# Kernel tuning notes

Hardware: AMD Instinct MI355X
Metric: run time of the kernel (lower is better)

## Reference

```python
import jax, jax.numpy as jnp
import numpy as np

N = 50000
E = 800000
IN_F = 128
OUT_F = 64
HEADS = 4
NEG_SLOPE = 0.2
EPS = 1e-8


def setup_inputs() -> dict:
    key = jax.random.key(0)
    k1, k2, k3, k4, k5 = jax.random.split(key, 5)
    x = jax.random.normal(k1, (N, IN_F), dtype=jnp.float32)
    edge_index = jax.random.randint(k2, (2, E), 0, N, dtype=jnp.int64)
    # xavier-uniform-like scales
    wb = float(np.sqrt(6.0 / (IN_F + OUT_F)))
    ab = float(np.sqrt(6.0 / (OUT_F + 1)))
    W = jax.random.uniform(k3, (HEADS, IN_F, OUT_F), dtype=jnp.float32, minval=-wb, maxval=wb)
    a_src = jax.random.uniform(k4, (HEADS, OUT_F, 1), dtype=jnp.float32, minval=-ab, maxval=ab)
    a_dst = jax.random.uniform(k5, (HEADS, OUT_F, 1), dtype=jnp.float32, minval=-ab, maxval=ab)
    return {"x": x, "edge_index": edge_index, "W": W, "a_src": a_src, "a_dst": a_dst}


def reference(x, edge_index, W, a_src, a_dst):
    n = x.shape[0]
    src, dst = edge_index[0], edge_index[1]
    # per-head projection: (H, N, F)
    Wh = jnp.einsum('ni,hif->hnf', x, W)
    e_src = jnp.einsum('hnf,hf->hn', Wh, a_src[..., 0])
    e_dst = jnp.einsum('hnf,hf->hn', Wh, a_dst[..., 0])
    e = jax.nn.leaky_relu(e_src[:, src] + e_dst[:, dst], NEG_SLOPE)  # (H, E)
    # edge softmax over destination; original initializes e_max to zeros,
    # so effective max is max(segment_max, 0)
    seg_max = jax.vmap(lambda eh: jax.ops.segment_max(eh, dst, num_segments=n))(e)
    e_max = jnp.maximum(seg_max, 0.0)
    exp_e = jnp.exp(e - e_max[:, dst])
    exp_sum = jax.vmap(lambda ee: jax.ops.segment_sum(ee, dst, num_segments=n))(exp_e)
    att = exp_e / (exp_sum[:, dst] + EPS)  # (H, E); dropout omitted (eval)
    # weighted scatter-add aggregation: (H, E, F) messages -> (H, N, F)
    msgs = att[..., None] * Wh[:, src]
    out = jax.vmap(lambda m: jax.ops.segment_sum(m, dst, num_segments=n))(msgs)
    # concat heads: (N, H*F)
    return out.transpose(1, 0, 2).reshape(n, -1)
```

## Files before the change

kernel.cpp:

```cpp
#include <hip/hip_runtime.h>
#include <hip/hip_bf16.h>

#define N_NODES 50000
#define E_EDGES 800000
#define IN_F    128
#define OUT_F   64
#define HEADS   4
#define HF      (HEADS * OUT_F)
#define NEG_SLOPE 0.2f
#define EPS     1e-8f
#define CAP     64
#define NB_INIT ((N_NODES + 255) / 256)

typedef __attribute__((ext_vector_type(8))) short bf16x8;
typedef __attribute__((ext_vector_type(4))) float f32x4;

__device__ __forceinline__ unsigned short f2bf(float f) {
    return __hip_bfloat16_raw(__float2bfloat16(f)).x;
}
__device__ __forceinline__ float bf2f(unsigned short u) {
    return __uint_as_float((unsigned)u << 16);
}

__global__ __launch_bounds__(256) void wcvt_kernel(
    const float* __restrict__ W,
    short* __restrict__ Wtb,
    int* __restrict__ cnt)
{
    const int i = blockIdx.x * 256 + threadIdx.x;
    if (i < N_NODES) cnt[i] = 0;
    if (i < HEADS * IN_F * OUT_F) {
        const int h  = i >> 13;
        const int fl = (i >> 7) & 63;
        const int k  = i & 127;
        Wtb[i] = (short)f2bf(W[h * (IN_F * OUT_F) + k * OUT_F + fl]);
    }
}

__global__ __launch_bounds__(256) void proj_kernel(
    const float* __restrict__ x,
    const short* __restrict__ Wtb,
    const float* __restrict__ a_src,
    const float* __restrict__ a_dst,
    const int* __restrict__ src,
    const int* __restrict__ dst,
    unsigned short* __restrict__ Whb,
    float* __restrict__ esrc,
    float* __restrict__ edst,
    int* __restrict__ cnt,
    int* __restrict__ csr)
{
    __shared__ short xs[16][136];
    __shared__ unsigned short ot[4][16][72];

    const int tid = threadIdx.x;
    const int n0 = blockIdx.x * 16;

    const int e  = blockIdx.x * 256 + tid;
    const int de = dst[e];
    const int se = src[e];

    {
        const int row = tid >> 4;
        const int kb = (tid & 15) * 8;
        const float* xp = x + (size_t)(n0 + row) * IN_F + kb;
        const float4 x0 = *(const float4*)(xp);
        const float4 x1 = *(const float4*)(xp + 4);
        bf16x8 v;
        v[0] = (short)f2bf(x0.x); v[1] = (short)f2bf(x0.y);
        v[2] = (short)f2bf(x0.z); v[3] = (short)f2bf(x0.w);
        v[4] = (short)f2bf(x1.x); v[5] = (short)f2bf(x1.y);
        v[6] = (short)f2bf(x1.z); v[7] = (short)f2bf(x1.w);
        *(bf16x8*)&xs[row][kb] = v;
    }
    __syncthreads();

    const int pos = atomicAdd(&cnt[de], 1);

    const int h = tid >> 6;
    const int lane = tid & 63;
    const int c = lane & 15;
    const int quad = lane >> 4;

    bf16x8 a[4];
#pragma unroll
    for (int ks = 0; ks < 4; ++ks)
        a[ks] = *(const bf16x8*)&xs[c][ks * 32 + quad * 8];

    f32x4 acc[4];
#pragma unroll
    for (int nt = 0; nt < 4; ++nt) acc[nt] = (f32x4){0.f, 0.f, 0.f, 0.f};

    const short* Wh_head = Wtb + (h << 13);
#pragma unroll
    for (int nt = 0; nt < 4; ++nt) {
        const short* wrow = Wh_head + ((nt * 16 + c) << 7) + (quad << 3);
#pragma unroll
        for (int ks = 0; ks < 4; ++ks) {
            const bf16x8 b = *(const bf16x8*)(wrow + (ks << 5));
            acc[nt] = __builtin_amdgcn_mfma_f32_16x16x32_bf16(a[ks], b, acc[nt], 0, 0, 0);
        }
    }

    float ps[4] = {0.f, 0.f, 0.f, 0.f};
    float pd[4] = {0.f, 0.f, 0.f, 0.f};
#pragma unroll
    for (int nt = 0; nt < 4; ++nt) {
        const float as = a_src[h * OUT_F + nt * 16 + c];
        const float ad = a_dst[h * OUT_F + nt * 16 + c];
#pragma unroll
        for (int r = 0; r < 4; ++r) {
            ps[r] += acc[nt][r] * as;
            pd[r] += acc[nt][r] * ad;
        }
    }
#pragma unroll
    for (int m = 1; m < 16; m <<= 1) {
#pragma unroll
        for (int r = 0; r < 4; ++r) {
            ps[r] += __shfl_xor(ps[r], m);
            pd[r] += __shfl_xor(pd[r], m);
        }
    }
    if (c == 0) {
#pragma unroll
        for (int r = 0; r < 4; ++r) {
            const int n = n0 + quad * 4 + r;
            esrc[n * HEADS + h] = ps[r];
            edst[n * HEADS + h] = pd[r];
        }
    }

#pragma unroll
    for (int nt = 0; nt < 4; ++nt) {
#pragma unroll
        for (int r = 0; r < 4; ++r)
            ot[h][quad * 4 + r][nt * 16 + c] = f2bf(acc[nt][r]);
    }
    {
        const int row = lane >> 2;
        const int co  = (lane & 3) * 16;
        unsigned short* gp = Whb + (size_t)(n0 + row) * HF + h * OUT_F + co;
        const unsigned short* sp = &ot[h][row][co];
        *(int4*)(gp)     = *(const int4*)(sp);
        *(int4*)(gp + 8) = *(const int4*)(sp + 8);
    }

    if (pos < CAP) __builtin_nontemporal_store(se, &csr[de * CAP + pos]);
}

__global__ __launch_bounds__(256) void aggregate_kernel(
    const int* __restrict__ cnt,
    const int* __restrict__ csr,
    const float* __restrict__ esrc,
    const float* __restrict__ edst,
    const unsigned short* __restrict__ Whb,
    float* __restrict__ out)
{
    __shared__ int   sb[4][64];
    __shared__ float pb[4][64][4];

    const int wid = threadIdx.x >> 6;
    const int lane = threadIdx.x & 63;
    const int d = blockIdx.x * 4 + wid;

    int deg = cnt[d];
    deg = deg > CAP ? CAP : deg;

    const float4 ed4 = *(const float4*)(edst + d * HEADS);
    const int h = lane >> 4;
    const unsigned short* wbase = Whb + (lane << 2);

    float l0 = 0.f, l1 = 0.f, l2 = 0.f, l3 = 0.f;
    if (lane < deg) {
        const int s = __builtin_nontemporal_load(&csr[d * CAP + lane]);
        const float4 es4 = *(const float4*)(esrc + s * HEADS);
        float v0 = es4.x + ed4.x; v0 = v0 > 0.f ? v0 : NEG_SLOPE * v0;
        float v1 = es4.y + ed4.y; v1 = v1 > 0.f ? v1 : NEG_SLOPE * v1;
        float v2 = es4.z + ed4.z; v2 = v2 > 0.f ? v2 : NEG_SLOPE * v2;
        float v3 = es4.w + ed4.w; v3 = v3 > 0.f ? v3 : NEG_SLOPE * v3;
        l0 = __expf(v0); l1 = __expf(v1); l2 = __expf(v2); l3 = __expf(v3);
        sb[wid][lane] = s;
        *(float4*)pb[wid][lane] = (float4){l0, l1, l2, l3};
    }

    float o0 = 0.f, o1 = 0.f, o2 = 0.f, o3 = 0.f;
    int i = 0;
    for (; i + 8 <= deg; i += 8) {
        int s[8];
#pragma unroll
        for (int j = 0; j < 8; ++j) s[j] = sb[wid][i + j];
        ushort4 w[8];
#pragma unroll
        for (int j = 0; j < 8; ++j)
            w[j] = *(const ushort4*)(wbase + (unsigned)s[j] * HF);
        float q[8];
#pragma unroll
        for (int j = 0; j < 8; ++j) q[j] = pb[wid][i + j][h];
#pragma unroll
        for (int j = 0; j < 8; ++j) {
            o0 += q[j] * bf2f(w[j].x);
            o1 += q[j] * bf2f(w[j].y);
            o2 += q[j] * bf2f(w[j].z);
            o3 += q[j] * bf2f(w[j].w);
        }
    }
    for (; i < deg; ++i) {
        const int s0 = sb[wid][i];
        const float q0 = pb[wid][i][h];
        const ushort4 w0 = *(const ushort4*)(wbase + (unsigned)s0 * HF);
        o0 += q0 * bf2f(w0.x);
        o1 += q0 * bf2f(w0.y);
        o2 += q0 * bf2f(w0.z);
        o3 += q0 * bf2f(w0.w);
    }

#pragma unroll
    for (int m = 1; m < 64; m <<= 1) {
        l0 += __shfl_xor(l0, m);
        l1 += __shfl_xor(l1, m);
        l2 += __shfl_xor(l2, m);
        l3 += __shfl_xor(l3, m);
    }
    const float lsum = (h == 0) ? l0 : (h == 1) ? l1 : (h == 2) ? l2 : l3;
    const float r = 1.f / (lsum + EPS);

    const f32x4 o4 = {o0 * r, o1 * r, o2 * r, o3 * r};
    __builtin_nontemporal_store(o4, (f32x4*)(out + (size_t)d * HF + (lane << 2)));
}

extern "C" void kernel_launch(void* const* d_in, const int* in_sizes, int n_in,
                              void* d_out, int out_size, void* d_ws, size_t ws_size,
                              hipStream_t stream) {
    const float* x      = (const float*)d_in[0];
    const int*   eidx   = (const int*)d_in[1];
    const float* W      = (const float*)d_in[2];
    const float* a_src  = (const float*)d_in[3];
    const float* a_dst  = (const float*)d_in[4];
    float* out = (float*)d_out;

    const int* src = eidx;
    const int* dst = eidx + E_EDGES;

    unsigned short* Whb = (unsigned short*)d_ws;
    float* esrc   = (float*)(Whb + (size_t)N_NODES * HF);
    float* edst   = esrc + (size_t)N_NODES * HEADS;
    int*   cnt    = (int*)(edst + (size_t)N_NODES * HEADS);
    int*   csr    = cnt + N_NODES;
    short* Wtb    = (short*)(csr + (size_t)N_NODES * CAP);

    wcvt_kernel<<<NB_INIT, 256, 0, stream>>>(W, Wtb, cnt);

    proj_kernel<<<N_NODES / 16, 256, 0, stream>>>(x, Wtb, a_src, a_dst, src, dst,
                                                  Whb, esrc, edst, cnt, csr);

    aggregate_kernel<<<N_NODES / 4, 256, 0, stream>>>(cnt, csr, esrc, edst, Whb, out);
}
```

Baseline: 193.1 us.

## Pad degree counters, store 16-bit CSR indices, unroll aggregation by 16

Each per-node degree counter now sits in its own 64-byte slot, so atomics on different nodes do not share cache lines. CSR source indices are stored as 16-bit values, which halves that buffer's footprint and relies on the node count fitting in 16 bits. The aggregation gather loop handles 16 neighbours per step with zero-padded shared entries instead of an 8-wide loop plus a tail loop, giving more loads in flight. The trade-offs are a larger counter array to zero, scattered sub-dword stores, and wasted gathers for low-degree nodes.

```diff
diff --git a/kernel.cpp b/kernel.cpp
--- a/kernel.cpp
+++ b/kernel.cpp
@@ -28,7 +28,11 @@
     int* __restrict__ cnt)
 {
     const int i = blockIdx.x * 256 + threadIdx.x;
-    if (i < N_NODES) cnt[i] = 0;
+    if (i < N_NODES) {
+        const int4 z = {0, 0, 0, 0};
+        int4* p = (int4*)(cnt + i * 16);
+        p[0] = z; p[1] = z; p[2] = z; p[3] = z;
+    }
     if (i < HEADS * IN_F * OUT_F) {
         const int h  = i >> 13;
         const int fl = (i >> 7) & 63;
@@ -48,7 +52,7 @@
     float* __restrict__ esrc,
     float* __restrict__ edst,
     int* __restrict__ cnt,
-    int* __restrict__ csr)
+    unsigned short* __restrict__ csr)
 {
     __shared__ short xs[16][136];
     __shared__ unsigned short ot[4][16][72];
@@ -75,7 +79,7 @@
     }
     __syncthreads();
 
-    const int pos = atomicAdd(&cnt[de], 1);
+    const int pos = atomicAdd(&cnt[de << 4], 1);
 
     const int h = tid >> 6;
     const int lane = tid & 63;
@@ -146,12 +150,13 @@
         *(int4*)(gp + 8) = *(const int4*)(sp + 8);
     }
 
-    if (pos < CAP) __builtin_nontemporal_store(se, &csr[de * CAP + pos]);
+    if (pos < CAP)
+        __builtin_nontemporal_store((unsigned short)se, &csr[(size_t)de * CAP + pos]);
 }
 
 __global__ __launch_bounds__(256) void aggregate_kernel(
     const int* __restrict__ cnt,
-    const int* __restrict__ csr,
+    const unsigned short* __restrict__ csr,
     const float* __restrict__ esrc,
     const float* __restrict__ edst,
     const unsigned short* __restrict__ Whb,
@@ -164,7 +169,7 @@
     const int lane = threadIdx.x & 63;
     const int d = blockIdx.x * 4 + wid;
 
-    int deg = cnt[d];
+    int deg = cnt[d << 4];
     deg = deg > CAP ? CAP : deg;
 
     const float4 ed4 = *(const float4*)(edst + d * HEADS);
@@ -172,47 +177,41 @@
     const unsigned short* wbase = Whb + (lane << 2);
 
     float l0 = 0.f, l1 = 0.f, l2 = 0.f, l3 = 0.f;
+    int sfill = 0;
+    float4 pfill = {0.f, 0.f, 0.f, 0.f};
     if (lane < deg) {
-        const int s = __builtin_nontemporal_load(&csr[d * CAP + lane]);
+        const int s = (int)__builtin_nontemporal_load(&csr[(size_t)d * CAP + lane]);
         const float4 es4 = *(const float4*)(esrc + s * HEADS);
         float v0 = es4.x + ed4.x; v0 = v0 > 0.f ? v0 : NEG_SLOPE * v0;
         float v1 = es4.y + ed4.y; v1 = v1 > 0.f ? v1 : NEG_SLOPE * v1;
         float v2 = es4.z + ed4.z; v2 = v2 > 0.f ? v2 : NEG_SLOPE * v2;
         float v3 = es4.w + ed4.w; v3 = v3 > 0.f ? v3 : NEG_SLOPE * v3;
         l0 = __expf(v0); l1 = __expf(v1); l2 = __expf(v2); l3 = __expf(v3);
-        sb[wid][lane] = s;
-        *(float4*)pb[wid][lane] = (float4){l0, l1, l2, l3};
-    }
+        sfill = s;
+        pfill = (float4){l0, l1, l2, l3};
+    }
+    sb[wid][lane] = sfill;
+    *(float4*)pb[wid][lane] = pfill;
 
     float o0 = 0.f, o1 = 0.f, o2 = 0.f, o3 = 0.f;
-    int i = 0;
-    for (; i + 8 <= deg; i += 8) {
-        int s[8];
-#pragma unroll
-        for (int j = 0; j < 8; ++j) s[j] = sb[wid][i + j];
-        ushort4 w[8];
-#pragma unroll
-        for (int j = 0; j < 8; ++j)
+    for (int i = 0; i < deg; i += 16) {
+        int s[16];
+#pragma unroll
+        for (int j = 0; j < 16; ++j) s[j] = sb[wid][i + j];
+        ushort4 w[16];
+#pragma unroll
+        for (int j = 0; j < 16; ++j)
             w[j] = *(const ushort4*)(wbase + (unsigned)s[j] * HF);
-        float q[8];
-#pragma unroll
-        for (int j = 0; j < 8; ++j) q[j] = pb[wid][i + j][h];
-#pragma unroll
-        for (int j = 0; j < 8; ++j) {
+        float q[16];
+#pragma unroll
+        for (int j = 0; j < 16; ++j) q[j] = pb[wid][i + j][h];
+#pragma unroll
+        for (int j = 0; j < 16; ++j) {
             o0 += q[j] * bf2f(w[j].x);
             o1 += q[j] * bf2f(w[j].y);
             o2 += q[j] * bf2f(w[j].z);
             o3 += q[j] * bf2f(w[j].w);
         }
-    }
-    for (; i < deg; ++i) {
-        const int s0 = sb[wid][i];
-        const float q0 = pb[wid][i][h];
-        const ushort4 w0 = *(const ushort4*)(wbase + (unsigned)s0 * HF);
-        o0 += q0 * bf2f(w0.x);
-        o1 += q0 * bf2f(w0.y);
-        o2 += q0 * bf2f(w0.z);
-        o3 += q0 * bf2f(w0.w);
     }
 
 #pragma unroll
@@ -246,7 +245,7 @@
     float* esrc   = (float*)(Whb + (size_t)N_NODES * HF);
     float* edst   = esrc + (size_t)N_NODES * HEADS;
     int*   cnt    = (int*)(edst + (size_t)N_NODES * HEADS);
-    int*   csr    = cnt + N_NODES;
+    unsigned short* csr = (unsigned short*)(cnt + (size_t)N_NODES * 16);
     short* Wtb    = (short*)(csr + (size_t)N_NODES * CAP);
 
     wcvt_kernel<<<NB_INIT, 256, 0, stream>>>(W, Wtb, cnt);
```

Measured after the change: 193.8 us. About the same (+0.3%).

## Fuse three kernels into one cooperative persistent kernel with grid syncs

Applied to the files above, without the earlier changes.

Replaces the three separate launches (weight convert/counter reset, projection, aggregation) with one cooperative kernel of 1024 persistent blocks that loops over tiles and separates phases with grid-wide syncs. The aim is to remove launch gaps and kernel-boundary drains between the phases. Nontemporal csr store/load are made plain so the CSR can stay in cache for the following phase. The trade-offs are grid.sync overhead, a fixed grid size limiting occupancy, and more shared memory per block; the old three-kernel path is kept as a fallback if the cooperative launch fails.

```diff
diff --git a/kernel.cpp b/kernel.cpp
--- a/kernel.cpp
+++ b/kernel.cpp
@@ -1,5 +1,8 @@
 #include <hip/hip_runtime.h>
 #include <hip/hip_bf16.h>
+#include <hip/hip_cooperative_groups.h>
+
+namespace cg = cooperative_groups;
 
 #define N_NODES 50000
 #define E_EDGES 800000
@@ -10,6 +13,9 @@
 #define NEG_SLOPE 0.2f
 #define EPS     1e-8f
 #define CAP     64
+#define NTILES  (N_NODES / 16)
+#define NAGG    (N_NODES / 4)
+#define NBLOCKS 1024
 #define NB_INIT ((N_NODES + 255) / 256)
 
 typedef __attribute__((ext_vector_type(8))) short bf16x8;
@@ -22,12 +28,11 @@
     return __uint_as_float((unsigned)u << 16);
 }
 
-__global__ __launch_bounds__(256) void wcvt_kernel(
-    const float* __restrict__ W,
-    short* __restrict__ Wtb,
+
+__device__ __forceinline__ void phase0_body(
+    int i, const float* __restrict__ W, short* __restrict__ Wtb,
     int* __restrict__ cnt)
 {
-    const int i = blockIdx.x * 256 + threadIdx.x;
     if (i < N_NODES) cnt[i] = 0;
     if (i < HEADS * IN_F * OUT_F) {
         const int h  = i >> 13;
@@ -37,26 +42,18 @@
     }
 }
 
-__global__ __launch_bounds__(256) void proj_kernel(
-    const float* __restrict__ x,
-    const short* __restrict__ Wtb,
-    const float* __restrict__ a_src,
-    const float* __restrict__ a_dst,
-    const int* __restrict__ src,
-    const int* __restrict__ dst,
-    unsigned short* __restrict__ Whb,
-    float* __restrict__ esrc,
-    float* __restrict__ edst,
-    int* __restrict__ cnt,
-    int* __restrict__ csr)
-{
-    __shared__ short xs[16][136];
-    __shared__ unsigned short ot[4][16][72];
-
-    const int tid = threadIdx.x;
-    const int n0 = blockIdx.x * 16;
-
-    const int e  = blockIdx.x * 256 + tid;
+__device__ __forceinline__ void proj_tile_body(
+    int t, int tid,
+    short (*xs)[136], unsigned short (*ot)[16][72],
+    const float* __restrict__ x, const short* __restrict__ Wtb,
+    const float* __restrict__ a_src, const float* __restrict__ a_dst,
+    const int* __restrict__ src, const int* __restrict__ dst,
+    unsigned short* __restrict__ Whb, float* __restrict__ esrc,
+    float* __restrict__ edst, int* __restrict__ cnt, int* __restrict__ csr)
+{
+    const int n0 = t * 16;
+
+    const int e  = t * 256 + tid;
     const int de = dst[e];
     const int se = src[e];
 
@@ -146,34 +143,28 @@
         *(int4*)(gp + 8) = *(const int4*)(sp + 8);
     }
 
-    if (pos < CAP) __builtin_nontemporal_store(se, &csr[de * CAP + pos]);
-}
-
-__global__ __launch_bounds__(256) void aggregate_kernel(
-    const int* __restrict__ cnt,
-    const int* __restrict__ csr,
-    const float* __restrict__ esrc,
-    const float* __restrict__ edst,
-    const unsigned short* __restrict__ Whb,
-    float* __restrict__ out)
-{
-    __shared__ int   sb[4][64];
-    __shared__ float pb[4][64][4];
-
-    const int wid = threadIdx.x >> 6;
-    const int lane = threadIdx.x & 63;
-    const int d = blockIdx.x * 4 + wid;
+    if (pos < CAP) csr[de * CAP + pos] = se;
+}
+
+__device__ __forceinline__ void agg_unit_body(
+    int u, int wid, int lane,
+    int (*sb)[64], float (*pb)[64][4],
+    const int* __restrict__ cnt, const int* __restrict__ csr,
+    const float* __restrict__ esrc, const float* __restrict__ edst,
+    const unsigned short* __restrict__ Whb, float* __restrict__ out)
+{
+    const int d = u * 4 + wid;
+    const int h = lane >> 4;
+    const unsigned short* wbase = Whb + (lane << 2);
 
     int deg = cnt[d];
     deg = deg > CAP ? CAP : deg;
 
     const float4 ed4 = *(const float4*)(edst + d * HEADS);
-    const int h = lane >> 4;
-    const unsigned short* wbase = Whb + (lane << 2);
 
     float l0 = 0.f, l1 = 0.f, l2 = 0.f, l3 = 0.f;
     if (lane < deg) {
-        const int s = __builtin_nontemporal_load(&csr[d * CAP + lane]);
+        const int s = csr[d * CAP + lane];
         const float4 es4 = *(const float4*)(esrc + s * HEADS);
         float v0 = es4.x + ed4.x; v0 = v0 > 0.f ? v0 : NEG_SLOPE * v0;
         float v1 = es4.y + ed4.y; v1 = v1 > 0.f ? v1 : NEG_SLOPE * v1;
@@ -223,10 +214,83 @@
         l3 += __shfl_xor(l3, m);
     }
     const float lsum = (h == 0) ? l0 : (h == 1) ? l1 : (h == 2) ? l2 : l3;
-    const float r = 1.f / (lsum + EPS);
-
-    const f32x4 o4 = {o0 * r, o1 * r, o2 * r, o3 * r};
+    const float rr = 1.f / (lsum + EPS);
+
+    const f32x4 o4 = {o0 * rr, o1 * rr, o2 * rr, o3 * rr};
     __builtin_nontemporal_store(o4, (f32x4*)(out + (size_t)d * HF + (lane << 2)));
+}
+
+__global__ __launch_bounds__(256, 4) void fused_kernel(
+    const float* __restrict__ x,
+    const float* __restrict__ W,
+    const float* __restrict__ a_src,
+    const float* __restrict__ a_dst,
+    const int* __restrict__ src,
+    const int* __restrict__ dst,
+    unsigned short* __restrict__ Whb,
+    float* __restrict__ esrc,
+    float* __restrict__ edst,
+    int* __restrict__ cnt,
+    int* __restrict__ csr,
+    short* __restrict__ Wtb,
+    float* __restrict__ out)
+{
+    cg::grid_group grid = cg::this_grid();
+
+    __shared__ short xs[16][136];
+    __shared__ unsigned short ot[4][16][72];
+    __shared__ int   sb[4][64];
+    __shared__ float pb[4][64][4];
+
+    const int tid = threadIdx.x;
+
+    for (int i = blockIdx.x * 256 + tid; i < N_NODES; i += NBLOCKS * 256)
+        phase0_body(i, W, Wtb, cnt);
+    __threadfence();
+    grid.sync();
+
+    for (int t = blockIdx.x; t < NTILES; t += NBLOCKS) {
+        proj_tile_body(t, tid, xs, ot, x, Wtb, a_src, a_dst, src, dst,
+                       Whb, esrc, edst, cnt, csr);
+        __syncthreads();
+    }
+    __threadfence();
+    grid.sync();
+
+    const int wid = tid >> 6;
+    const int lane = tid & 63;
+    for (int u = blockIdx.x; u < NAGG; u += NBLOCKS)
+        agg_unit_body(u, wid, lane, sb, pb, cnt, csr, esrc, edst, Whb, out);
+}
+
+__global__ __launch_bounds__(256) void wcvt_kernel(
+    const float* __restrict__ W, short* __restrict__ Wtb, int* __restrict__ cnt)
+{
+    phase0_body(blockIdx.x * 256 + threadIdx.x, W, Wtb, cnt);
+}
+
+__global__ __launch_bounds__(256) void proj_kernel(
+    const float* __restrict__ x, const short* __restrict__ Wtb,
+    const float* __restrict__ a_src, const float* __restrict__ a_dst,
+    const int* __restrict__ src, const int* __restrict__ dst,
+    unsigned short* __restrict__ Whb, float* __restrict__ esrc,
+    float* __restrict__ edst, int* __restrict__ cnt, int* __restrict__ csr)
+{
+    __shared__ short xs[16][136];
+    __shared__ unsigned short ot[4][16][72];
+    proj_tile_body(blockIdx.x, threadIdx.x, xs, ot, x, Wtb, a_src, a_dst,
+                   src, dst, Whb, esrc, edst, cnt, csr);
+}
+
+__global__ __launch_bounds__(256) void aggregate_kernel(
+    const int* __restrict__ cnt, const int* __restrict__ csr,
+    const float* __restrict__ esrc, const float* __restrict__ edst,
+    const unsigned short* __restrict__ Whb, float* __restrict__ out)
+{
+    __shared__ int   sb[4][64];
+    __shared__ float pb[4][64][4];
+    agg_unit_body(blockIdx.x, threadIdx.x >> 6, threadIdx.x & 63,
+                  sb, pb, cnt, csr, esrc, edst, Whb, out);
 }
 
 extern "C" void kernel_launch(void* const* d_in, const int* in_sizes, int n_in,
@@ -249,10 +313,19 @@
     int*   csr    = cnt + N_NODES;
     short* Wtb    = (short*)(csr + (size_t)N_NODES * CAP);
 
-    wcvt_kernel<<<NB_INIT, 256, 0, stream>>>(W, Wtb, cnt);
-
-    proj_kernel<<<N_NODES / 16, 256, 0, stream>>>(x, Wtb, a_src, a_dst, src, dst,
-                                                  Whb, esrc, edst, cnt, csr);
-
-    aggregate_kernel<<<N_NODES / 4, 256, 0, stream>>>(cnt, csr, esrc, edst, Whb, out);
-}
+    void* args[] = {
+        (void*)&x, (void*)&W, (void*)&a_src, (void*)&a_dst,
+        (void*)&src, (void*)&dst,
+        (void*)&Whb, (void*)&esrc, (void*)&edst,
+        (void*)&cnt, (void*)&csr, (void*)&Wtb, (void*)&out
+    };
+    hipError_t err = hipLaunchCooperativeKernel((const void*)fused_kernel,
+                                                dim3(NBLOCKS), dim3(256),
+                                                args, 0, stream);
+    if (err != hipSuccess) {
+        wcvt_kernel<<<NB_INIT, 256, 0, stream>>>(W, Wtb, cnt);
+        proj_kernel<<<NTILES, 256, 0, stream>>>(x, Wtb, a_src, a_dst, src, dst,
+                                                Whb, esrc, edst, cnt, csr);
+        aggregate_kernel<<<NAGG, 256, 0, stream>>>(cnt, csr, esrc, edst, Whb, out);
+    }
+}
```

New measurement: 572.5 us. +196.4%, slower.
